# Kernel optimization log

Hardware: AMD Instinct MI355X
Metric: run time of the kernel (lower is better)

The kernel has to match this reference:

```python
import jax, jax.numpy as jnp
import numpy as np

NUM_HEADS = 16
THETA = 10000.0

def _rope(t, token_ids, theta):
    # t: [B, H, S, Dk]; token_ids: [S]
    d_k = t.shape[-1]
    inv_freq = theta ** (-jnp.arange(0, d_k, 2, dtype=jnp.float32) / d_k)  # [Dk/2]
    ang = token_ids.astype(jnp.float32)[:, None] * inv_freq[None, :]       # [S, Dk/2]
    cos, sin = jnp.cos(ang), jnp.sin(ang)
    x1, x2 = t[..., ::2], t[..., 1::2]
    r1 = x1 * cos - x2 * sin
    r2 = x1 * sin + x2 * cos
    return jnp.stack([r1, r2], axis=-1).reshape(t.shape)

def setup_inputs() -> dict:
    key = jax.random.key(0)
    ks = jax.random.split(key, 5)
    d_model = 1024
    scale = 0.02
    return {
        "x": jax.random.normal(ks[0], (4, 2048, d_model), dtype=jnp.float32),
        "token_ids": jnp.arange(2048, dtype=jnp.int32),
        "Wq": jax.random.normal(ks[1], (d_model, d_model), dtype=jnp.float32) * scale,
        "Wk": jax.random.normal(ks[2], (d_model, d_model), dtype=jnp.float32) * scale,
        "Wv": jax.random.normal(ks[3], (d_model, d_model), dtype=jnp.float32) * scale,
        "Wo": jax.random.normal(ks[4], (d_model, d_model), dtype=jnp.float32) * scale,
    }

def reference(x, token_ids, Wq, Wk, Wv, Wo):
    B, S, D = x.shape
    H = NUM_HEADS
    Dk = D // H
    def split_heads(t):
        return t.reshape(B, S, H, Dk).transpose(0, 2, 1, 3)  # [B,H,S,Dk]
    q = split_heads(x @ Wq.T)
    k = split_heads(x @ Wk.T)
    v = split_heads(x @ Wv.T)
    q = _rope(q, token_ids, THETA)
    k = _rope(k, token_ids, THETA)
    scores = jnp.einsum("bhqd,bhkd->bhqk", q, k) / jnp.sqrt(jnp.float32(Dk))
    causal = jnp.tril(jnp.ones((S, S), dtype=bool))
    scores = jnp.where(causal, scores, jnp.float32(-1e9))
    attn = jax.nn.softmax(scores, axis=-1)
    out = jnp.einsum("bhqk,bhkd->bhqd", attn, v)
    out = out.transpose(0, 2, 1, 3).reshape(B, S, H * Dk)
    return out @ Wo.T
```

## Files before the change

### kernel.cpp

```cpp
#include <hip/hip_runtime.h>

#define BATCH 4
#define SLEN 2048
#define DMODEL 1024
#define NHEADS 16
#define DK 64
#define MROWS (BATCH * SLEN)
#define NQB 16
#define SCALE_LOG2E 0.1803368801111731f

typedef short bf16x8 __attribute__((ext_vector_type(8)));
typedef unsigned short u16x4 __attribute__((ext_vector_type(4)));
typedef float f32x4 __attribute__((ext_vector_type(4)));

__device__ __forceinline__ unsigned short f2bf(float f) {
    unsigned u = __float_as_uint(f);
    unsigned r = u + 0x7FFFu + ((u >> 16) & 1u);
    return (unsigned short)(r >> 16);
}

__device__ __forceinline__ unsigned pkbf(float a, float b) {
    unsigned r;
    asm volatile("v_cvt_pk_bf16_f32 %0, %1, %2" : "=v"(r) : "v"(a), "v"(b));
    return r;
}

__device__ __forceinline__ void gload_lds16(const void* g, void* l) {
    __builtin_amdgcn_global_load_lds(
        (const __attribute__((address_space(1))) void*)g,
        (__attribute__((address_space(3))) void*)l, 16, 0, 0);
}

__global__ void cvt_f32_bf16(const float* __restrict__ in, unsigned short* __restrict__ out, int n) {
    int i = (blockIdx.x * blockDim.x + threadIdx.x) * 4;
    if (i >= n) return;
    float4 v = *reinterpret_cast<const float4*>(in + i);
    u16x4 o;
    o[0] = f2bf(v.x); o[1] = f2bf(v.y); o[2] = f2bf(v.z); o[3] = f2bf(v.w);
    *reinterpret_cast<u16x4*>(out + i) = o;
}

__global__ void cvt_w_all(const float* __restrict__ w0, const float* __restrict__ w1,
                          const float* __restrict__ w2, const float* __restrict__ w3,
                          unsigned short* __restrict__ o0, unsigned short* __restrict__ o1,
                          unsigned short* __restrict__ o2, unsigned short* __restrict__ o3) {
    int z = blockIdx.y;
    const float* src = (z == 0) ? w0 : (z == 1) ? w1 : (z == 2) ? w2 : w3;
    unsigned short* dst = (z == 0) ? o0 : (z == 1) ? o1 : (z == 2) ? o2 : o3;
    int i = (blockIdx.x * blockDim.x + threadIdx.x) * 4;
    float4 v = *reinterpret_cast<const float4*>(src + i);
    u16x4 o;
    o[0] = f2bf(v.x); o[1] = f2bf(v.y); o[2] = f2bf(v.z); o[3] = f2bf(v.w);
    *reinterpret_cast<u16x4*>(dst + i) = o;
}

__global__ void rope_table(const int* __restrict__ tok, float* __restrict__ cs, float* __restrict__ sn) {
    int idx = blockIdx.x * blockDim.x + threadIdx.x;
    if (idx >= SLEN * 32) return;
    int s = idx >> 5, fi = idx & 31;
    float invf = powf(10000.0f, -(float)(2 * fi) / 64.0f);
    float ang = (float)tok[s] * invf;
    cs[idx] = cosf(ang);
    sn[idx] = sinf(ang);
}

__global__ __launch_bounds__(256) void qkv_gemm(
    const unsigned short* __restrict__ X,
    const unsigned short* __restrict__ Wq,
    const unsigned short* __restrict__ Wk,
    const unsigned short* __restrict__ Wv,
    const float* __restrict__ cs_tab, const float* __restrict__ sn_tab,
    unsigned short* __restrict__ Q, unsigned short* __restrict__ K,
    unsigned short* __restrict__ VT)
{
    __shared__ alignas(16) unsigned short As[128 * 64];
    __shared__ alignas(16) unsigned short Bs[3][64 * 64];
    const int tid = threadIdx.x, lane = tid & 63, wave = tid >> 6;
    const int ln = lane & 15, kq = lane >> 4;
    const int wr = wave >> 1, wc = wave & 1;
    const int m0 = blockIdx.x * 128;
    const int n0 = blockIdx.y * 64;
    const unsigned short* Ws[3] = {Wq, Wk, Wv};

    f32x4 acc[3][4][2];
#pragma unroll
    for (int z = 0; z < 3; z++)
#pragma unroll
        for (int a = 0; a < 4; a++)
#pragma unroll
            for (int b = 0; b < 2; b++) acc[z][a][b] = (f32x4){0.f, 0.f, 0.f, 0.f};

    for (int k0 = 0; k0 < DMODEL; k0 += 64) {
        if (k0) __syncthreads();
#pragma unroll
        for (int i = 0; i < 4; i++) {
            int s = i * 256 + tid;
            int r = s >> 3;
            int u = (s & 7) ^ (r & 7);
            gload_lds16(X + (size_t)(m0 + r) * DMODEL + k0 + u * 8, &As[(i * 256 + wave * 64) * 8]);
        }
#pragma unroll
        for (int z = 0; z < 3; z++)
#pragma unroll
            for (int i = 0; i < 2; i++) {
                int s = i * 256 + tid;
                int r = s >> 3;
                int u = (s & 7) ^ (r & 7);
                gload_lds16(Ws[z] + (size_t)(n0 + r) * DMODEL + k0 + u * 8,
                            &Bs[z][(i * 256 + wave * 64) * 8]);
            }
        __syncthreads();

        bf16x8 af[4][2];
#pragma unroll
        for (int mt = 0; mt < 4; mt++) {
            int row = wr * 64 + mt * 16 + ln;
#pragma unroll
            for (int kc = 0; kc < 2; kc++) {
                int u = (kc * 4 + kq) ^ (row & 7);
                af[mt][kc] = *reinterpret_cast<const bf16x8*>(&As[row * 64 + u * 8]);
            }
        }
#pragma unroll
        for (int z = 0; z < 3; z++) {
            bf16x8 bfr[2][2];
#pragma unroll
            for (int nt = 0; nt < 2; nt++) {
                int row = wc * 32 + nt * 16 + ln;
#pragma unroll
                for (int kc = 0; kc < 2; kc++) {
                    int u = (kc * 4 + kq) ^ (row & 7);
                    bfr[nt][kc] = *reinterpret_cast<const bf16x8*>(&Bs[z][row * 64 + u * 8]);
                }
            }
            __builtin_amdgcn_s_setprio(1);
#pragma unroll
            for (int kc = 0; kc < 2; kc++)
#pragma unroll
                for (int mt = 0; mt < 4; mt++)
#pragma unroll
                    for (int nt = 0; nt < 2; nt++)
                        acc[z][mt][nt] = __builtin_amdgcn_mfma_f32_16x16x32_bf16(
                            af[mt][kc], bfr[nt][kc], acc[z][mt][nt], 0, 0, 0);
            __builtin_amdgcn_s_setprio(0);
        }
    }

    int m0w = m0 + wr * 64;
    int n0w = n0 + wc * 32;
#pragma unroll
    for (int z = 0; z < 2; z++) {
        unsigned short* dst = z ? K : Q;
#pragma unroll
        for (int nt = 0; nt < 2; nt++) {
            int n = n0w + nt * 16 + ln;
            int h = n >> 6, d = n & 63;
            int fi = d >> 1;
#pragma unroll
            for (int mt = 0; mt < 4; mt++) {
#pragma unroll
                for (int j = 0; j < 4; j++) {
                    int m = m0w + mt * 16 + kq * 4 + j;
                    int b = m >> 11, s = m & (SLEN - 1);
                    float v = acc[z][mt][nt][j];
                    float c = cs_tab[s * 32 + fi];
                    float si = sn_tab[s * 32 + fi];
                    float p = __shfl_xor(v, 1);
                    v = (d & 1) ? (p * si + v * c) : (v * c - p * si);
                    if (z == 0) v *= SCALE_LOG2E;
                    dst[(((size_t)(b * NHEADS + h) * SLEN + s) << 6) + d] = f2bf(v);
                }
            }
        }
    }
#pragma unroll
    for (int nt = 0; nt < 2; nt++) {
        int n = n0w + nt * 16 + ln;
        int h = n >> 6, d = n & 63;
#pragma unroll
        for (int mt = 0; mt < 4; mt++) {
#pragma unroll
            for (int j = 0; j < 4; j++) {
                int m = m0w + mt * 16 + kq * 4 + j;
                int b = m >> 11, s = m & (SLEN - 1);
                VT[((size_t)(b * NHEADS + h) * DK + d) * SLEN + s] = f2bf(acc[2][mt][nt][j]);
            }
        }
    }
}

__device__ __forceinline__ void gemm128_core_sb(
    const unsigned short* __restrict__ A, const unsigned short* __restrict__ B,
    int m0, int n0, int tid, f32x4 (&acc)[4][4],
    unsigned short* As, unsigned short* Bs)
{
    int lane = tid & 63, wave = tid >> 6;
    int ln = lane & 15, kq = lane >> 4;
    int wr = wave >> 1, wc = wave & 1;
#pragma unroll
    for (int a = 0; a < 4; a++)
#pragma unroll
        for (int b = 0; b < 4; b++) acc[a][b] = (f32x4){0.f, 0.f, 0.f, 0.f};

    for (int k0 = 0; k0 < DMODEL; k0 += 64) {
        if (k0) __syncthreads();
#pragma unroll
        for (int i = 0; i < 4; i++) {
            int s = i * 256 + tid;
            int r = s >> 3;
            int u = (s & 7) ^ (r & 7);
            gload_lds16(A + (size_t)(m0 + r) * DMODEL + k0 + u * 8, &As[(i * 256 + wave * 64) * 8]);
            gload_lds16(B + (size_t)(n0 + r) * DMODEL + k0 + u * 8, &Bs[(i * 256 + wave * 64) * 8]);
        }
        __syncthreads();

        bf16x8 af[4][2], bfr[4][2];
#pragma unroll
        for (int mt = 0; mt < 4; mt++) {
            int row = wr * 64 + mt * 16 + ln;
#pragma unroll
            for (int kc = 0; kc < 2; kc++) {
                int u = (kc * 4 + kq) ^ (row & 7);
                af[mt][kc] = *reinterpret_cast<const bf16x8*>(&As[row * 64 + u * 8]);
            }
        }
#pragma unroll
        for (int nt = 0; nt < 4; nt++) {
            int row = wc * 64 + nt * 16 + ln;
#pragma unroll
            for (int kc = 0; kc < 2; kc++) {
                int u = (kc * 4 + kq) ^ (row & 7);
                bfr[nt][kc] = *reinterpret_cast<const bf16x8*>(&Bs[row * 64 + u * 8]);
            }
        }
        __builtin_amdgcn_s_setprio(1);
#pragma unroll
        for (int kc = 0; kc < 2; kc++)
#pragma unroll
            for (int mt = 0; mt < 4; mt++)
#pragma unroll
                for (int nt = 0; nt < 4; nt++)
                    acc[mt][nt] = __builtin_amdgcn_mfma_f32_16x16x32_bf16(af[mt][kc], bfr[nt][kc], acc[mt][nt], 0, 0, 0);
        __builtin_amdgcn_s_setprio(0);
    }
}

__global__ __launch_bounds__(256, 4) void attn_kernel(
    const unsigned short* __restrict__ Q, const unsigned short* __restrict__ K,
    const unsigned short* __restrict__ VT, unsigned short* __restrict__ O)
{
    __shared__ alignas(16) unsigned short Kt[2][4096];
    __shared__ alignas(16) unsigned short Vt[2][4096];

    int tid = threadIdx.x, lane = tid & 63, wave = tid >> 6;
    int ln = lane & 15, kq = lane >> 4;
    int qb = blockIdx.x;
    int h = blockIdx.y, b = blockIdx.z;
    size_t headoff = ((size_t)b * NHEADS + h) * SLEN * DK;
    const unsigned short* Qh = Q + headoff;
    const unsigned short* Kh = K + headoff;
    const unsigned short* Vh = VT + headoff;

    auto stage = [&](int buf, int t) {
        int kv0 = t << 6;
#pragma unroll
        for (int i = 0; i < 2; i++) {
            int s = i * 256 + tid;
            int r = s >> 3;
            int cb = (s & 7) ^ (r & 7);
            int rp = ((r >> 5) << 5) | (((r >> 2) & 3) << 3) | (((r >> 4) & 1) << 2) | (r & 3);
            gload_lds16(Kh + (size_t)(kv0 + rp) * DK + cb * 8,
                        &Kt[buf][(i * 256 + wave * 64) * 8]);
            gload_lds16(Vh + (size_t)r * SLEN + kv0 + cb * 8,
                        &Vt[buf][(i * 256 + wave * 64) * 8]);
        }
    };

    for (int sid = 0; sid < 2; sid++) {
        int qs = sid ? qb : (NQB - 1 - qb);
        int q0 = qs * 128 + wave * 32;

        bf16x8 aq[2][2];
#pragma unroll
        for (int mt = 0; mt < 2; mt++)
#pragma unroll
            for (int kc = 0; kc < 2; kc++)
                aq[mt][kc] = *reinterpret_cast<const bf16x8*>(
                    Qh + (size_t)(q0 + mt * 16 + ln) * DK + kc * 32 + kq * 8);

        f32x4 oacc[2][4];
#pragma unroll
        for (int mt = 0; mt < 2; mt++)
#pragma unroll
            for (int nt = 0; nt < 4; nt++) oacc[mt][nt] = (f32x4){0.f, 0.f, 0.f, 0.f};
        float m_r[2] = {-1e30f, -1e30f};
        float l_r[2] = {0.f, 0.f};

        int tmax_w = (q0 + 31) >> 6;
        int ntiles = 2 * qs + 2;

        stage(0, 0);
        __syncthreads();

        for (int t = 0; t < ntiles; t++) {
            int buf = t & 1;
            if (t + 1 < ntiles) stage(buf ^ 1, t + 1);

            if (t <= tmax_w) {
                int kv0 = t << 6;
                f32x4 sacc[2][4];
#pragma unroll
                for (int mt = 0; mt < 2; mt++)
#pragma unroll
                    for (int nt = 0; nt < 4; nt++) sacc[mt][nt] = (f32x4){0.f, 0.f, 0.f, 0.f};
                __builtin_amdgcn_s_setprio(1);
#pragma unroll
                for (int nt = 0; nt < 4; nt++) {
                    int rr = nt * 16 + ln;
#pragma unroll
                    for (int kc = 0; kc < 2; kc++) {
                        int unit = (kc * 4 + kq) ^ (rr & 7);
                        bf16x8 bk = *reinterpret_cast<const bf16x8*>(&Kt[buf][rr * 64 + unit * 8]);
#pragma unroll
                        for (int mt = 0; mt < 2; mt++)
                            sacc[mt][nt] = __builtin_amdgcn_mfma_f32_16x16x32_bf16(bk, aq[mt][kc], sacc[mt][nt], 0, 0, 0);
                    }
                }
                __builtin_amdgcn_s_setprio(0);

                if (kv0 + 63 > q0) {
#pragma unroll
                    for (int mt = 0; mt < 2; mt++) {
                        int q = q0 + mt * 16 + ln;
#pragma unroll
                        for (int nt = 0; nt < 4; nt++)
#pragma unroll
                            for (int j = 0; j < 4; j++) {
                                int k = kv0 + (nt >> 1) * 32 + kq * 8 + (nt & 1) * 4 + j;
                                if (k > q) sacc[mt][nt][j] = -1e30f;
                            }
                    }
                }

                float mloc[2];
#pragma unroll
                for (int mt = 0; mt < 2; mt++) {
                    f32x4 m4 = sacc[mt][0];
#pragma unroll
                    for (int nt = 1; nt < 4; nt++) {
                        m4[0] = fmaxf(m4[0], sacc[mt][nt][0]);
                        m4[1] = fmaxf(m4[1], sacc[mt][nt][1]);
                        m4[2] = fmaxf(m4[2], sacc[mt][nt][2]);
                        m4[3] = fmaxf(m4[3], sacc[mt][nt][3]);
                    }
                    mloc[mt] = fmaxf(fmaxf(m4[0], m4[1]), fmaxf(m4[2], m4[3]));
                }
#pragma unroll
                for (int mt = 0; mt < 2; mt++) {
                    mloc[mt] = fmaxf(mloc[mt], __shfl_xor(mloc[mt], 16));
                    mloc[mt] = fmaxf(mloc[mt], __shfl_xor(mloc[mt], 32));
                }

                bool needscale = !__all((mloc[0] <= m_r[0] + 8.0f) && (mloc[1] <= m_r[1] + 8.0f));
                float so[2] = {1.f, 1.f};
                if (needscale) {
#pragma unroll
                    for (int mt = 0; mt < 2; mt++) {
                        float mn = fmaxf(m_r[mt], mloc[mt]);
                        so[mt] = exp2f(m_r[mt] - mn);
                        m_r[mt] = mn;
                    }
                }

                float rs[2] = {0.f, 0.f};
#pragma unroll
                for (int mt = 0; mt < 2; mt++)
#pragma unroll
                    for (int nt = 0; nt < 4; nt++)
#pragma unroll
                        for (int j = 0; j < 4; j++) {
                            float p = exp2f(sacc[mt][nt][j] - m_r[mt]);
                            sacc[mt][nt][j] = p;
                            rs[mt] += p;
                        }
#pragma unroll
                for (int mt = 0; mt < 2; mt++) {
                    rs[mt] += __shfl_xor(rs[mt], 16);
                    rs[mt] += __shfl_xor(rs[mt], 32);
                    l_r[mt] = l_r[mt] * so[mt] + rs[mt];
                }

                if (needscale) {
                    float so_o[2][4];
#pragma unroll
                    for (int mt = 0; mt < 2; mt++)
#pragma unroll
                        for (int j = 0; j < 4; j++)
                            so_o[mt][j] = __shfl(so[mt], kq * 4 + j, 16);
#pragma unroll
                    for (int mt = 0; mt < 2; mt++)
#pragma unroll
                        for (int nt = 0; nt < 4; nt++)
#pragma unroll
                            for (int j = 0; j < 4; j++)
                                oacc[mt][nt][j] *= so_o[mt][j];
                }

                bf16x8 pa[2][2];
#pragma unroll
                for (int mt = 0; mt < 2; mt++)
#pragma unroll
                    for (int kc = 0; kc < 2; kc++) {
                        union { unsigned u[4]; bf16x8 v; } r;
                        r.u[0] = pkbf(sacc[mt][2 * kc][0], sacc[mt][2 * kc][1]);
                        r.u[1] = pkbf(sacc[mt][2 * kc][2], sacc[mt][2 * kc][3]);
                        r.u[2] = pkbf(sacc[mt][2 * kc + 1][0], sacc[mt][2 * kc + 1][1]);
                        r.u[3] = pkbf(sacc[mt][2 * kc + 1][2], sacc[mt][2 * kc + 1][3]);
                        pa[mt][kc] = r.v;
                    }

                __builtin_amdgcn_s_setprio(1);
#pragma unroll
                for (int nt = 0; nt < 4; nt++) {
                    int rr = nt * 16 + ln;
#pragma unroll
                    for (int kc = 0; kc < 2; kc++) {
                        int unit = (kc * 4 + kq) ^ (rr & 7);
                        bf16x8 bv = *reinterpret_cast<const bf16x8*>(&Vt[buf][rr * 64 + unit * 8]);
#pragma unroll
                        for (int mt = 0; mt < 2; mt++)
                            oacc[mt][nt] = __builtin_amdgcn_mfma_f32_16x16x32_bf16(pa[mt][kc], bv, oacc[mt][nt], 0, 0, 0);
                    }
                }
                __builtin_amdgcn_s_setprio(0);
            }
            __syncthreads();
        }

        float lo[2][4];
#pragma unroll
        for (int mt = 0; mt < 2; mt++)
#pragma unroll
            for (int j = 0; j < 4; j++)
                lo[mt][j] = __shfl(l_r[mt], kq * 4 + j, 16);
#pragma unroll
        for (int mt = 0; mt < 2; mt++)
#pragma unroll
            for (int nt = 0; nt < 4; nt++)
#pragma unroll
                for (int j = 0; j < 4; j++) {
                    int row = q0 + mt * 16 + kq * 4 + j;
                    float v = oacc[mt][nt][j] / lo[mt][j];
                    O[((size_t)b * SLEN + row) * DMODEL + h * 64 + nt * 16 + ln] = f2bf(v);
                }
        __syncthreads();
    }
}

__global__ __launch_bounds__(256) void out_gemm(
    const unsigned short* __restrict__ A, const unsigned short* __restrict__ Wo,
    float* __restrict__ out)
{
    __shared__ alignas(16) unsigned short As[128 * 64];
    __shared__ alignas(16) unsigned short Bs[128 * 64];
    int tid = threadIdx.x, lane = tid & 63, wave = tid >> 6;
    int ln = lane & 15, kq = lane >> 4;
    int wr = wave >> 1, wc = wave & 1;
    int m0 = blockIdx.x * 128;
    int n0 = blockIdx.y * 128;

    f32x4 acc[4][4];
    gemm128_core_sb(A, Wo, m0, n0, tid, acc, As, Bs);

    int m0w = m0 + wr * 64, n0w = n0 + wc * 64;
#pragma unroll
    for (int mt = 0; mt < 4; mt++)
#pragma unroll
        for (int nt = 0; nt < 4; nt++)
#pragma unroll
            for (int j = 0; j < 4; j++) {
                int m = m0w + mt * 16 + kq * 4 + j;
                int n = n0w + nt * 16 + ln;
                out[(size_t)m * DMODEL + n] = acc[mt][nt][j];
            }
}

extern "C" void kernel_launch(void* const* d_in, const int* in_sizes, int n_in,
                              void* d_out, int out_size, void* d_ws, size_t ws_size,
                              hipStream_t stream) {
    const float* x  = (const float*)d_in[0];
    const int* tok  = (const int*)d_in[1];
    const float* wq = (const float*)d_in[2];
    const float* wk = (const float*)d_in[3];
    const float* wv = (const float*)d_in[4];
    const float* wo = (const float*)d_in[5];
    float* out = (float*)d_out;

    const size_t XB_OFF = 0;
    const size_t WQ_OFF = 16777216;
    const size_t WK_OFF = 18874368;
    const size_t WV_OFF = 20971520;
    const size_t WO_OFF = 23068672;
    const size_t Q_OFF  = 25165824;
    const size_t K_OFF  = 41943040;
    const size_t VT_OFF = 58720256;
    const size_t O_OFF  = 75497472;
    const size_t CS_OFF = 92274688;
    const size_t SN_OFF = 92536832;
    const size_t WS_NEEDED = 92798976;
    if (ws_size < WS_NEEDED) return;

    char* ws = (char*)d_ws;
    unsigned short* Xb  = (unsigned short*)(ws + XB_OFF);
    unsigned short* Wqb = (unsigned short*)(ws + WQ_OFF);
    unsigned short* Wkb = (unsigned short*)(ws + WK_OFF);
    unsigned short* Wvb = (unsigned short*)(ws + WV_OFF);
    unsigned short* Wob = (unsigned short*)(ws + WO_OFF);
    unsigned short* Qb  = (unsigned short*)(ws + Q_OFF);
    unsigned short* Kb  = (unsigned short*)(ws + K_OFF);
    unsigned short* VTb = (unsigned short*)(ws + VT_OFF);
    unsigned short* Ob  = (unsigned short*)(ws + O_OFF);
    float* cs_tab = (float*)(ws + CS_OFF);
    float* sn_tab = (float*)(ws + SN_OFF);

    cvt_f32_bf16<<<8192, 256, 0, stream>>>(x, Xb, MROWS * DMODEL);
    cvt_w_all<<<dim3(1024, 4), 256, 0, stream>>>(wq, wk, wv, wo, Wqb, Wkb, Wvb, Wob);
    rope_table<<<256, 256, 0, stream>>>(tok, cs_tab, sn_tab);

    qkv_gemm<<<dim3(MROWS / 128, DMODEL / 64, 1), 256, 0, stream>>>(
        Xb, Wqb, Wkb, Wvb, cs_tab, sn_tab, Qb, Kb, VTb);

    attn_kernel<<<dim3(SLEN / 256, NHEADS, BATCH), 256, 0, stream>>>(Qb, Kb, VTb, Ob);

    out_gemm<<<dim3(MROWS / 128, DMODEL / 128, 1), 256, 0, stream>>>(Ob, Wob, out);
}
```

Before: 221.4 us.

## Process paired causal query blocks concurrently with 8 waves sharing KV tiles

The attention kernel now runs 512 threads (8 waves), each owning 16 query rows in both the long and the short causal block. It makes a single pass over KV tiles, so one staged K/V tile serves both query blocks instead of running two sequential passes that each restage K/V. The intent is to halve KV staging traffic, balance work across waves and add more waves per block for latency hiding. In exchange, MFMA work per wave is smaller (one 16-row strip per instruction group instead of two), and register use and occupancy limits change with the 512-thread launch bound.

```diff
diff --git a/kernel.cpp b/kernel.cpp
--- a/kernel.cpp
+++ b/kernel.cpp
@@ -245,7 +245,7 @@
     }
 }
 
-__global__ __launch_bounds__(256, 4) void attn_kernel(
+__global__ __launch_bounds__(512, 4) void attn_kernel(
     const unsigned short* __restrict__ Q, const unsigned short* __restrict__ K,
     const unsigned short* __restrict__ VT, unsigned short* __restrict__ O)
 {
@@ -263,197 +263,169 @@
 
     auto stage = [&](int buf, int t) {
         int kv0 = t << 6;
-#pragma unroll
-        for (int i = 0; i < 2; i++) {
-            int s = i * 256 + tid;
-            int r = s >> 3;
-            int cb = (s & 7) ^ (r & 7);
-            int rp = ((r >> 5) << 5) | (((r >> 2) & 3) << 3) | (((r >> 4) & 1) << 2) | (r & 3);
-            gload_lds16(Kh + (size_t)(kv0 + rp) * DK + cb * 8,
-                        &Kt[buf][(i * 256 + wave * 64) * 8]);
-            gload_lds16(Vh + (size_t)r * SLEN + kv0 + cb * 8,
-                        &Vt[buf][(i * 256 + wave * 64) * 8]);
-        }
+        int s = tid;
+        int r = s >> 3;
+        int cb = (s & 7) ^ (r & 7);
+        int rp = ((r >> 5) << 5) | (((r >> 2) & 3) << 3) | (((r >> 4) & 1) << 2) | (r & 3);
+        gload_lds16(Kh + (size_t)(kv0 + rp) * DK + cb * 8, &Kt[buf][(wave * 64) * 8]);
+        gload_lds16(Vh + (size_t)r * SLEN + kv0 + cb * 8, &Vt[buf][(wave * 64) * 8]);
     };
 
-    for (int sid = 0; sid < 2; sid++) {
-        int qs = sid ? qb : (NQB - 1 - qb);
-        int q0 = qs * 128 + wave * 32;
-
-        bf16x8 aq[2][2];
-#pragma unroll
-        for (int mt = 0; mt < 2; mt++)
-#pragma unroll
-            for (int kc = 0; kc < 2; kc++)
-                aq[mt][kc] = *reinterpret_cast<const bf16x8*>(
-                    Qh + (size_t)(q0 + mt * 16 + ln) * DK + kc * 32 + kq * 8);
-
-        f32x4 oacc[2][4];
-#pragma unroll
-        for (int mt = 0; mt < 2; mt++)
-#pragma unroll
-            for (int nt = 0; nt < 4; nt++) oacc[mt][nt] = (f32x4){0.f, 0.f, 0.f, 0.f};
-        float m_r[2] = {-1e30f, -1e30f};
-        float l_r[2] = {0.f, 0.f};
-
-        int tmax_w = (q0 + 31) >> 6;
-        int ntiles = 2 * qs + 2;
-
-        stage(0, 0);
+    const int q0A = (NQB - 1 - qb) * 128 + wave * 16;
+    const int q0B = qb * 128 + wave * 16;
+    const int ntA = 2 * (NQB - 1 - qb) + 2;
+    const int tmaxA = (q0A + 15) >> 6;
+    const int tmaxB = (q0B + 15) >> 6;
+
+    bf16x8 aqA[2], aqB[2];
+#pragma unroll
+    for (int kc = 0; kc < 2; kc++) {
+        aqA[kc] = *reinterpret_cast<const bf16x8*>(Qh + (size_t)(q0A + ln) * DK + kc * 32 + kq * 8);
+        aqB[kc] = *reinterpret_cast<const bf16x8*>(Qh + (size_t)(q0B + ln) * DK + kc * 32 + kq * 8);
+    }
+
+    f32x4 oaccA[4], oaccB[4];
+#pragma unroll
+    for (int nt = 0; nt < 4; nt++) {
+        oaccA[nt] = (f32x4){0.f, 0.f, 0.f, 0.f};
+        oaccB[nt] = (f32x4){0.f, 0.f, 0.f, 0.f};
+    }
+    float mA = -1e30f, lA = 0.f, mB = -1e30f, lB = 0.f;
+
+    stage(0, 0);
+    __syncthreads();
+
+    for (int t = 0; t < ntA; t++) {
+        int buf = t & 1;
+        if (t + 1 < ntA) stage(buf ^ 1, t + 1);
+        int kv0 = t << 6;
+
+        auto strip = [&](int q0, bf16x8 (&aq)[2], f32x4 (&oacc)[4], float& m_r, float& l_r) {
+            f32x4 sacc[4];
+#pragma unroll
+            for (int nt = 0; nt < 4; nt++) sacc[nt] = (f32x4){0.f, 0.f, 0.f, 0.f};
+            __builtin_amdgcn_s_setprio(1);
+#pragma unroll
+            for (int nt = 0; nt < 4; nt++) {
+                int rr = nt * 16 + ln;
+#pragma unroll
+                for (int kc = 0; kc < 2; kc++) {
+                    int unit = (kc * 4 + kq) ^ (rr & 7);
+                    bf16x8 bk = *reinterpret_cast<const bf16x8*>(&Kt[buf][rr * 64 + unit * 8]);
+                    sacc[nt] = __builtin_amdgcn_mfma_f32_16x16x32_bf16(bk, aq[kc], sacc[nt], 0, 0, 0);
+                }
+            }
+            __builtin_amdgcn_s_setprio(0);
+
+            if (kv0 + 63 > q0) {
+                int q = q0 + ln;
+#pragma unroll
+                for (int nt = 0; nt < 4; nt++)
+#pragma unroll
+                    for (int j = 0; j < 4; j++) {
+                        int k = kv0 + (nt >> 1) * 32 + kq * 8 + (nt & 1) * 4 + j;
+                        if (k > q) sacc[nt][j] = -1e30f;
+                    }
+            }
+
+            f32x4 m4 = sacc[0];
+#pragma unroll
+            for (int nt = 1; nt < 4; nt++) {
+                m4[0] = fmaxf(m4[0], sacc[nt][0]);
+                m4[1] = fmaxf(m4[1], sacc[nt][1]);
+                m4[2] = fmaxf(m4[2], sacc[nt][2]);
+                m4[3] = fmaxf(m4[3], sacc[nt][3]);
+            }
+            float mloc = fmaxf(fmaxf(m4[0], m4[1]), fmaxf(m4[2], m4[3]));
+            mloc = fmaxf(mloc, __shfl_xor(mloc, 16));
+            mloc = fmaxf(mloc, __shfl_xor(mloc, 32));
+
+            bool needscale = !__all(mloc <= m_r + 8.0f);
+            float so = 1.f;
+            if (needscale) {
+                float mn = fmaxf(m_r, mloc);
+                so = exp2f(m_r - mn);
+                m_r = mn;
+            }
+
+            float rs = 0.f;
+#pragma unroll
+            for (int nt = 0; nt < 4; nt++)
+#pragma unroll
+                for (int j = 0; j < 4; j++) {
+                    float p = exp2f(sacc[nt][j] - m_r);
+                    sacc[nt][j] = p;
+                    rs += p;
+                }
+            rs += __shfl_xor(rs, 16);
+            rs += __shfl_xor(rs, 32);
+            l_r = l_r * so + rs;
+
+            if (needscale) {
+                float so_o[4];
+#pragma unroll
+                for (int j = 0; j < 4; j++) so_o[j] = __shfl(so, kq * 4 + j, 16);
+#pragma unroll
+                for (int nt = 0; nt < 4; nt++)
+#pragma unroll
+                    for (int j = 0; j < 4; j++)
+                        oacc[nt][j] *= so_o[j];
+            }
+
+            bf16x8 pa[2];
+#pragma unroll
+            for (int kc = 0; kc < 2; kc++) {
+                union { unsigned u[4]; bf16x8 v; } r;
+                r.u[0] = pkbf(sacc[2 * kc][0], sacc[2 * kc][1]);
+                r.u[1] = pkbf(sacc[2 * kc][2], sacc[2 * kc][3]);
+                r.u[2] = pkbf(sacc[2 * kc + 1][0], sacc[2 * kc + 1][1]);
+                r.u[3] = pkbf(sacc[2 * kc + 1][2], sacc[2 * kc + 1][3]);
+                pa[kc] = r.v;
+            }
+
+            __builtin_amdgcn_s_setprio(1);
+#pragma unroll
+            for (int nt = 0; nt < 4; nt++) {
+                int rr = nt * 16 + ln;
+#pragma unroll
+                for (int kc = 0; kc < 2; kc++) {
+                    int unit = (kc * 4 + kq) ^ (rr & 7);
+                    bf16x8 bv = *reinterpret_cast<const bf16x8*>(&Vt[buf][rr * 64 + unit * 8]);
+                    oacc[nt] = __builtin_amdgcn_mfma_f32_16x16x32_bf16(pa[kc], bv, oacc[nt], 0, 0, 0);
+                }
+            }
+            __builtin_amdgcn_s_setprio(0);
+        };
+
+        if (t <= tmaxA) strip(q0A, aqA, oaccA, mA, lA);
+        if (t <= tmaxB) strip(q0B, aqB, oaccB, mB, lB);
+
         __syncthreads();
-
-        for (int t = 0; t < ntiles; t++) {
-            int buf = t & 1;
-            if (t + 1 < ntiles) stage(buf ^ 1, t + 1);
-
-            if (t <= tmax_w) {
-                int kv0 = t << 6;
-                f32x4 sacc[2][4];
-#pragma unroll
-                for (int mt = 0; mt < 2; mt++)
-#pragma unroll
-                    for (int nt = 0; nt < 4; nt++) sacc[mt][nt] = (f32x4){0.f, 0.f, 0.f, 0.f};
-                __builtin_amdgcn_s_setprio(1);
-#pragma unroll
-                for (int nt = 0; nt < 4; nt++) {
-                    int rr = nt * 16 + ln;
-#pragma unroll
-                    for (int kc = 0; kc < 2; kc++) {
-                        int unit = (kc * 4 + kq) ^ (rr & 7);
-                        bf16x8 bk = *reinterpret_cast<const bf16x8*>(&Kt[buf][rr * 64 + unit * 8]);
-#pragma unroll
-                        for (int mt = 0; mt < 2; mt++)
-                            sacc[mt][nt] = __builtin_amdgcn_mfma_f32_16x16x32_bf16(bk, aq[mt][kc], sacc[mt][nt], 0, 0, 0);
-                    }
-                }
-                __builtin_amdgcn_s_setprio(0);
-
-                if (kv0 + 63 > q0) {
-#pragma unroll
-                    for (int mt = 0; mt < 2; mt++) {
-                        int q = q0 + mt * 16 + ln;
-#pragma unroll
-                        for (int nt = 0; nt < 4; nt++)
-#pragma unroll
-                            for (int j = 0; j < 4; j++) {
-                                int k = kv0 + (nt >> 1) * 32 + kq * 8 + (nt & 1) * 4 + j;
-                                if (k > q) sacc[mt][nt][j] = -1e30f;
-                            }
-                    }
-                }
-
-                float mloc[2];
-#pragma unroll
-                for (int mt = 0; mt < 2; mt++) {
-                    f32x4 m4 = sacc[mt][0];
-#pragma unroll
-                    for (int nt = 1; nt < 4; nt++) {
-                        m4[0] = fmaxf(m4[0], sacc[mt][nt][0]);
-                        m4[1] = fmaxf(m4[1], sacc[mt][nt][1]);
-                        m4[2] = fmaxf(m4[2], sacc[mt][nt][2]);
-                        m4[3] = fmaxf(m4[3], sacc[mt][nt][3]);
-                    }
-                    mloc[mt] = fmaxf(fmaxf(m4[0], m4[1]), fmaxf(m4[2], m4[3]));
-                }
-#pragma unroll
-                for (int mt = 0; mt < 2; mt++) {
-                    mloc[mt] = fmaxf(mloc[mt], __shfl_xor(mloc[mt], 16));
-                    mloc[mt] = fmaxf(mloc[mt], __shfl_xor(mloc[mt], 32));
-                }
-
-                bool needscale = !__all((mloc[0] <= m_r[0] + 8.0f) && (mloc[1] <= m_r[1] + 8.0f));
-                float so[2] = {1.f, 1.f};
-                if (needscale) {
-#pragma unroll
-                    for (int mt = 0; mt < 2; mt++) {
-                        float mn = fmaxf(m_r[mt], mloc[mt]);
-                        so[mt] = exp2f(m_r[mt] - mn);
-                        m_r[mt] = mn;
-                    }
-                }
-
-                float rs[2] = {0.f, 0.f};
-#pragma unroll
-                for (int mt = 0; mt < 2; mt++)
-#pragma unroll
-                    for (int nt = 0; nt < 4; nt++)
-#pragma unroll
-                        for (int j = 0; j < 4; j++) {
-                            float p = exp2f(sacc[mt][nt][j] - m_r[mt]);
-                            sacc[mt][nt][j] = p;
-                            rs[mt] += p;
-                        }
-#pragma unroll
-                for (int mt = 0; mt < 2; mt++) {
-                    rs[mt] += __shfl_xor(rs[mt], 16);
-                    rs[mt] += __shfl_xor(rs[mt], 32);
-                    l_r[mt] = l_r[mt] * so[mt] + rs[mt];
-                }
-
-                if (needscale) {
-                    float so_o[2][4];
-#pragma unroll
-                    for (int mt = 0; mt < 2; mt++)
-#pragma unroll
-                        for (int j = 0; j < 4; j++)
-                            so_o[mt][j] = __shfl(so[mt], kq * 4 + j, 16);
-#pragma unroll
-                    for (int mt = 0; mt < 2; mt++)
-#pragma unroll
-                        for (int nt = 0; nt < 4; nt++)
-#pragma unroll
-                            for (int j = 0; j < 4; j++)
-                                oacc[mt][nt][j] *= so_o[mt][j];
-                }
-
-                bf16x8 pa[2][2];
-#pragma unroll
-                for (int mt = 0; mt < 2; mt++)
-#pragma unroll
-                    for (int kc = 0; kc < 2; kc++) {
-                        union { unsigned u[4]; bf16x8 v; } r;
-                        r.u[0] = pkbf(sacc[mt][2 * kc][0], sacc[mt][2 * kc][1]);
-                        r.u[1] = pkbf(sacc[mt][2 * kc][2], sacc[mt][2 * kc][3]);
-                        r.u[2] = pkbf(sacc[mt][2 * kc + 1][0], sacc[mt][2 * kc + 1][1]);
-                        r.u[3] = pkbf(sacc[mt][2 * kc + 1][2], sacc[mt][2 * kc + 1][3]);
-                        pa[mt][kc] = r.v;
-                    }
-
-                __builtin_amdgcn_s_setprio(1);
-#pragma unroll
-                for (int nt = 0; nt < 4; nt++) {
-                    int rr = nt * 16 + ln;
-#pragma unroll
-                    for (int kc = 0; kc < 2; kc++) {
-                        int unit = (kc * 4 + kq) ^ (rr & 7);
-                        bf16x8 bv = *reinterpret_cast<const bf16x8*>(&Vt[buf][rr * 64 + unit * 8]);
-#pragma unroll
-                        for (int mt = 0; mt < 2; mt++)
-                            oacc[mt][nt] = __builtin_amdgcn_mfma_f32_16x16x32_bf16(pa[mt][kc], bv, oacc[mt][nt], 0, 0, 0);
-                    }
-                }
-                __builtin_amdgcn_s_setprio(0);
-            }
-            __syncthreads();
-        }
-
-        float lo[2][4];
-#pragma unroll
-        for (int mt = 0; mt < 2; mt++)
-#pragma unroll
-            for (int j = 0; j < 4; j++)
-                lo[mt][j] = __shfl(l_r[mt], kq * 4 + j, 16);
-#pragma unroll
-        for (int mt = 0; mt < 2; mt++)
-#pragma unroll
-            for (int nt = 0; nt < 4; nt++)
-#pragma unroll
-                for (int j = 0; j < 4; j++) {
-                    int row = q0 + mt * 16 + kq * 4 + j;
-                    float v = oacc[mt][nt][j] / lo[mt][j];
-                    O[((size_t)b * SLEN + row) * DMODEL + h * 64 + nt * 16 + ln] = f2bf(v);
-                }
-        __syncthreads();
+    }
+
+    {
+        float lo[4];
+#pragma unroll
+        for (int j = 0; j < 4; j++) lo[j] = __shfl(lA, kq * 4 + j, 16);
+#pragma unroll
+        for (int nt = 0; nt < 4; nt++)
+#pragma unroll
+            for (int j = 0; j < 4; j++) {
+                int row = q0A + kq * 4 + j;
+                O[((size_t)b * SLEN + row) * DMODEL + h * 64 + nt * 16 + ln] = f2bf(oaccA[nt][j] / lo[j]);
+            }
+    }
+    {
+        float lo[4];
+#pragma unroll
+        for (int j = 0; j < 4; j++) lo[j] = __shfl(lB, kq * 4 + j, 16);
+#pragma unroll
+        for (int nt = 0; nt < 4; nt++)
+#pragma unroll
+            for (int j = 0; j < 4; j++) {
+                int row = q0B + kq * 4 + j;
+                O[((size_t)b * SLEN + row) * DMODEL + h * 64 + nt * 16 + ln] = f2bf(oaccB[nt][j] / lo[j]);
+            }
     }
 }
 
@@ -530,7 +502,7 @@
     qkv_gemm<<<dim3(MROWS / 128, DMODEL / 64, 1), 256, 0, stream>>>(
         Xb, Wqb, Wkb, Wvb, cs_tab, sn_tab, Qb, Kb, VTb);
 
-    attn_kernel<<<dim3(SLEN / 256, NHEADS, BATCH), 256, 0, stream>>>(Qb, Kb, VTb, Ob);
+    attn_kernel<<<dim3(SLEN / 256, NHEADS, BATCH), 512, 0, stream>>>(Qb, Kb, VTb, Ob);
 
     out_gemm<<<dim3(MROWS / 128, DMODEL / 128, 1), 256, 0, stream>>>(Ob, Wob, out);
 }
```

Result: faster. 210.9 us, median of 3 (-4.8%).
